# Kernel optimization log

Measured on AMD Instinct MI355X. Metric: run time of the kernel, lower is better.

The kernel has to match this reference:

```python
import jax, jax.numpy as jnp
import numpy as np


def _gcn_conv(x, src, dst, W, b, num_nodes, deg_inv_sqrt):
    # PyG GCNConv: h = x @ W, then normalized scatter-add over edges (incl. self loops), + bias
    h = x @ W  # [N, d_out]
    norm = deg_inv_sqrt[src] * deg_inv_sqrt[dst]  # [E']
    msg = h[src] * norm[:, None]  # gather + scale, [E', d_out]
    out = jax.ops.segment_sum(msg, dst, num_segments=num_nodes)  # scatter-add to targets
    return out + b


def reference(x, edge_index, W1, b1, W2, b2, num_nodes):
    src0, dst0 = edge_index[0], edge_index[1]
    loop = jnp.arange(num_nodes, dtype=edge_index.dtype)
    # add self loops (PyG default add_self_loops=True)
    src = jnp.concatenate([src0, loop])
    dst = jnp.concatenate([dst0, loop])
    # symmetric normalization D^{-1/2} (A+I) D^{-1/2}, degree from self-looped graph
    deg = jax.ops.segment_sum(jnp.ones_like(src, dtype=x.dtype), dst, num_segments=num_nodes)
    deg_inv_sqrt = jnp.where(deg > 0, jax.lax.rsqrt(jnp.maximum(deg, 1)), 0.0).astype(x.dtype)

    z = jax.nn.relu(_gcn_conv(x, src, dst, W1, b1, num_nodes, deg_inv_sqrt))
    z = jax.nn.relu(_gcn_conv(z, src, dst, W2, b2, num_nodes, deg_inv_sqrt))
    return z


def setup_inputs() -> dict:
    key = jax.random.key(0)
    k1, k2, k3, k4 = jax.random.split(key, 4)
    N, E, D, H = 50000, 1600000, 128, 128
    x = jax.random.normal(k1, (N, D), dtype=jnp.float32)
    edge_index = jax.random.randint(k2, (2, E), 0, N, dtype=jnp.int64)
    s = 1.0 / np.sqrt(D)
    W1 = jax.random.normal(k3, (D, H), dtype=jnp.float32) * s
    W2 = jax.random.normal(k4, (H, H), dtype=jnp.float32) * s
    return {
        "x": x,
        "edge_index": edge_index,
        "W1": W1,
        "b1": jnp.zeros((H,), jnp.float32),
        "W2": W2,
        "b2": jnp.zeros((H,), jnp.float32),
        "num_nodes": N,
    }
```

## Files before the change

### kernel.cpp

```cpp
#include <hip/hip_runtime.h>

#define FD 128
#define BSH 7
#define CH 2048
#define CHT 8
#define KMAX 512
#define SCAP 8192

typedef __attribute__((ext_vector_type(8))) short bf16x8;
typedef __attribute__((ext_vector_type(4))) float f32x4;

__device__ inline unsigned bfr(float f) {
    unsigned u = __float_as_uint(f);
    return (u + 0x7FFF + ((u >> 16) & 1)) >> 16;
}
__device__ inline float uplo(unsigned p) { return __uint_as_float(p << 16); }
__device__ inline float uphi(unsigned p) { return __uint_as_float(p & 0xFFFF0000u); }


__global__ __launch_bounds__(256) void partition_kernel(
        const int* __restrict__ src, const int* __restrict__ dst,
        int* __restrict__ lstartG, int* __restrict__ total,
        int* __restrict__ pairs, int E, int K) {
    __shared__ int lcnt[KMAX];
    __shared__ int lstart[KMAX];
    __shared__ int sm[256];
    __shared__ int staged[CH];
    int t = threadIdx.x;
    int base = blockIdx.x * CH;
    int n = min(CH, E - base);

    lcnt[t] = 0; lcnt[t + 256] = 0;
    __syncthreads();

    int pk[CHT]; int bn[CHT];
    #pragma unroll
    for (int j = 0; j < CHT; ++j) {
        int i = t + j * 256;
        bn[j] = -1;
        if (i < n) {
            int d = dst[base + i];
            int s = src[base + i];
            bn[j] = d >> BSH;
            pk[j] = ((d & ((1 << BSH) - 1)) << 17) | s;
            atomicAdd(&lcnt[bn[j]], 1);
        }
    }
    __syncthreads();

    int c0 = lcnt[2 * t], c1 = lcnt[2 * t + 1];
    int s2 = c0 + c1;
    sm[t] = s2;
    __syncthreads();
    for (int off = 1; off < 256; off <<= 1) {
        int add = (t >= off) ? sm[t - off] : 0;
        __syncthreads();
        sm[t] += add;
        __syncthreads();
    }
    int ex = sm[t] - s2;
    lstart[2 * t] = ex;     lstart[2 * t + 1] = ex + c0;
    lcnt[2 * t]   = ex;     lcnt[2 * t + 1]   = ex + c0;
    __syncthreads();

    #pragma unroll
    for (int j = 0; j < CHT; ++j) {
        if (bn[j] >= 0) {
            int pos = atomicAdd(&lcnt[bn[j]], 1);
            staged[pos] = pk[j];
        }
    }
    __syncthreads();

    for (int i = t; i < n; i += 256)
        pairs[base + i] = staged[i];

    size_t lrow = (size_t)blockIdx.x * (K + 1);
    for (int b = t; b < K; b += 256) {
        lstartG[lrow + b] = lstart[b];
        int c = lcnt[b] - lstart[b];
        if (c) atomicAdd(&total[b], c);
    }
    if (t == 0) lstartG[lrow + K] = n;
}

__global__ __launch_bounds__(512) void totscan_kernel(
        const int* __restrict__ total, int* __restrict__ bbase,
        int* __restrict__ rp, int K, int E, int N) {
    __shared__ int sm[512];
    int t = threadIdx.x;
    int v = (t < K) ? total[t] : 0;
    sm[t] = v;
    __syncthreads();
    for (int off = 1; off < 512; off <<= 1) {
        int add = (t >= off) ? sm[t - off] : 0;
        __syncthreads();
        sm[t] += add;
        __syncthreads();
    }
    if (t < K) bbase[t] = sm[t] - v;
    if (t == 0) { bbase[K] = E; rp[N] = E; }
}

__global__ __launch_bounds__(256) void build_kernel(
        const int* __restrict__ pairs, const int* __restrict__ lstartG,
        const int* __restrict__ bbase, int* __restrict__ rp,
        float* __restrict__ dis, int* __restrict__ col, int N, int PB, int K) {
    __shared__ int staged[SCAP];
    __shared__ int lcnt[1 << BSH];
    __shared__ int lsum[1 << BSH];
    __shared__ int lbase[1 << BSH];
    __shared__ int sm[256];
    int b = blockIdx.x;
    int t = threadIdx.x;
    int nbase = b << BSH;
    int nn = min(1 << BSH, N - nbase);
    int beg = bbase[b];
    int cnt = bbase[b + 1] - beg;

    int fp[4], fl0[4], flen[4];
    int nf = 0, mysum = 0;
    for (int p = t; p < PB; p += 256) {
        size_t lrow = (size_t)p * (K + 1);
        int l0 = lstartG[lrow + b];
        int l1 = lstartG[lrow + b + 1];
        fp[nf] = p; fl0[nf] = l0; flen[nf] = l1 - l0;
        mysum += l1 - l0;
        ++nf;
    }
    sm[t] = mysum;
    __syncthreads();
    for (int off = 1; off < 256; off <<= 1) {
        int add = (t >= off) ? sm[t - off] : 0;
        __syncthreads();
        sm[t] += add;
        __syncthreads();
    }
    int o = sm[t] - mysum;

    if (t < 128) lcnt[t] = 0;

    if (cnt <= SCAP) {
        for (int f = 0; f < nf; ++f) {
            int gbase = fp[f] * CH + fl0[f];
            for (int i = 0; i < flen[f]; ++i) staged[o + i] = pairs[gbase + i];
            o += flen[f];
        }
        __syncthreads();
        for (int i = t; i < cnt; i += 256) atomicAdd(&lcnt[staged[i] >> 17], 1);
    } else {
        __syncthreads();
        for (int f = 0; f < nf; ++f) {
            int gbase = fp[f] * CH + fl0[f];
            for (int i = 0; i < flen[f]; ++i)
                atomicAdd(&lcnt[pairs[gbase + i] >> 17], 1);
        }
    }
    __syncthreads();

    if (t < 128) lsum[t] = lcnt[t];
    __syncthreads();
    for (int off = 1; off < 128; off <<= 1) {
        int add = (t < 128 && t >= off) ? lsum[t - off] : 0;
        __syncthreads();
        if (t < 128) lsum[t] += add;
        __syncthreads();
    }
    if (t < 128) {
        int excl = beg + lsum[t] - lcnt[t];
        lbase[t] = excl;
        if (t < nn) {
            rp[nbase + t] = excl;
            dis[nbase + t] = rsqrtf((float)(lcnt[t] + 1));
        }
    }
    __syncthreads();
    if (t < 128) lcnt[t] = lbase[t];
    __syncthreads();

    if (cnt <= SCAP) {
        for (int i = t; i < cnt; i += 256) {
            int p = staged[i];
            int pos = atomicAdd(&lcnt[p >> 17], 1);
            col[pos] = p & 0x1FFFF;
        }
    } else {
        for (int f = 0; f < nf; ++f) {
            int gbase = fp[f] * CH + fl0[f];
            for (int i = 0; i < flen[f]; ++i) {
                int p = pairs[gbase + i];
                int pos = atomicAdd(&lcnt[p >> 17], 1);
                col[pos] = p & 0x1FFFF;
            }
        }
    }
}


__global__ void wt_kernel(const float* __restrict__ W1, unsigned short* __restrict__ W1T,
                          const float* __restrict__ W2, unsigned short* __restrict__ W2T) {
    int k = blockIdx.x & (FD - 1);
    int n = threadIdx.x;
    if (blockIdx.x < FD) W1T[n * FD + k] = (unsigned short)bfr(W1[k * FD + n]);
    else                 W2T[n * FD + k] = (unsigned short)bfr(W2[k * FD + n]);
}


#define APAD 8
#define ASTR (FD + APAD)

template <bool A32>
__device__ void gemm_body(const void* __restrict__ Ap,
                          const unsigned short* __restrict__ WT,
                          const float* __restrict__ dis,
                          unsigned short* __restrict__ C, int M) {
    __shared__ unsigned short As[128 * ASTR];
    __shared__ unsigned short Bs[128 * ASTR];
    int tid = threadIdx.x;
    int lane = tid & 63;
    int wave = tid >> 6;
    int quad = lane >> 4;
    int l16 = lane & 15;
    int rowBase = blockIdx.x * 128;

    #pragma unroll
    for (int p = 0; p < 8; ++p) {
        int r = p * 16 + (tid >> 4);
        int cq = (tid & 15) * 8;
        int gr = rowBase + r;
        uint4 v = make_uint4(0u, 0u, 0u, 0u);
        if (A32) {
            if (gr < M) {
                const float* a = (const float*)Ap + (size_t)gr * FD + cq;
                float4 f0 = *(const float4*)a;
                float4 f1 = *(const float4*)(a + 4);
                v.x = bfr(f0.x) | (bfr(f0.y) << 16);
                v.y = bfr(f0.z) | (bfr(f0.w) << 16);
                v.z = bfr(f1.x) | (bfr(f1.y) << 16);
                v.w = bfr(f1.z) | (bfr(f1.w) << 16);
            }
        } else {
            if (gr < M) v = *(const uint4*)((const unsigned short*)Ap + (size_t)gr * FD + cq);
        }
        *(uint4*)&As[r * ASTR + cq] = v;
        *(uint4*)&Bs[r * ASTR + cq] = *(const uint4*)&WT[(size_t)r * FD + cq];
    }
    __syncthreads();

    int m0 = wave * 32;
    f32x4 acc[2][8] = {};
    #pragma unroll
    for (int kt = 0; kt < 4; ++kt) {
        int ko = kt * 32 + quad * 8;
        bf16x8 a0 = *(bf16x8*)&As[(m0 + l16) * ASTR + ko];
        bf16x8 a1 = *(bf16x8*)&As[(m0 + 16 + l16) * ASTR + ko];
        #pragma unroll
        for (int n = 0; n < 8; ++n) {
            bf16x8 b = *(bf16x8*)&Bs[(n * 16 + l16) * ASTR + ko];
            acc[0][n] = __builtin_amdgcn_mfma_f32_16x16x32_bf16(a0, b, acc[0][n], 0, 0, 0);
            acc[1][n] = __builtin_amdgcn_mfma_f32_16x16x32_bf16(a1, b, acc[1][n], 0, 0, 0);
        }
    }

    #pragma unroll
    for (int ms = 0; ms < 2; ++ms) {
        #pragma unroll
        for (int r = 0; r < 4; ++r) {
            int grow = rowBase + m0 + ms * 16 + quad * 4 + r;
            if (grow < M) {
                float dv = dis[grow];
                #pragma unroll
                for (int n = 0; n < 8; ++n) {
                    C[(size_t)grow * FD + n * 16 + l16] =
                        (unsigned short)bfr(dv * acc[ms][n][r]);
                }
            }
        }
    }
}

__global__ __launch_bounds__(256) void gemm_mfma_f32(
        const float* __restrict__ A, const unsigned short* __restrict__ WT,
        const float* __restrict__ dis, unsigned short* __restrict__ C, int M) {
    gemm_body<true>(A, WT, dis, C, M);
}

__global__ __launch_bounds__(256) void gemm_mfma_bf16(
        const unsigned short* __restrict__ A, const unsigned short* __restrict__ WT,
        const float* __restrict__ dis, unsigned short* __restrict__ C, int M) {
    gemm_body<false>(A, WT, dis, C, M);
}


__global__ __launch_bounds__(256) void agg_kernel(
        const unsigned* __restrict__ h, const float* __restrict__ dis,
        const int* __restrict__ rp, const int* __restrict__ col,
        const float2* __restrict__ bias, void* __restrict__ out, int N, int obf) {
    int v = blockIdx.x * 4 + threadIdx.y;
    v = __builtin_amdgcn_readfirstlane(v);
    if (v >= N) return;
    int t = threadIdx.x;
    float dv = dis[v];
    size_t vb = (size_t)v * 64 + t;
    unsigned hp = h[vb];
    float2 acc;
    acc.x = uplo(hp); acc.y = uphi(hp);
    int e = rp[v];
    int end = rp[v + 1];

    for (; e + 16 <= end; e += 16) {
        int u[16];
        #pragma unroll
        for (int j = 0; j < 16; ++j) u[j] = col[e + j];
        unsigned p[16];
        #pragma unroll
        for (int j = 0; j < 16; ++j) p[j] = h[(size_t)u[j] * 64 + t];
        #pragma unroll
        for (int j = 0; j < 16; ++j) {
            acc.x += uplo(p[j]); acc.y += uphi(p[j]);
        }
    }
    for (; e + 4 <= end; e += 4) {
        int u0 = col[e], u1 = col[e + 1], u2 = col[e + 2], u3 = col[e + 3];
        unsigned p0 = h[(size_t)u0 * 64 + t];
        unsigned p1 = h[(size_t)u1 * 64 + t];
        unsigned p2 = h[(size_t)u2 * 64 + t];
        unsigned p3 = h[(size_t)u3 * 64 + t];
        acc.x += uplo(p0); acc.y += uphi(p0);
        acc.x += uplo(p1); acc.y += uphi(p1);
        acc.x += uplo(p2); acc.y += uphi(p2);
        acc.x += uplo(p3); acc.y += uphi(p3);
    }
    for (; e < end; ++e) {
        unsigned p = h[(size_t)col[e] * 64 + t];
        acc.x += uplo(p); acc.y += uphi(p);
    }

    float2 bb = bias[t];
    float2 r;
    r.x = fmaxf(fmaf(dv, acc.x, bb.x), 0.0f);
    r.y = fmaxf(fmaf(dv, acc.y, bb.y), 0.0f);
    if (obf) {
        ((unsigned*)out)[vb] = bfr(r.x) | (bfr(r.y) << 16);
    } else {
        ((float2*)out)[vb] = r;
    }
}


extern "C" void kernel_launch(void* const* d_in, const int* in_sizes, int n_in,
                              void* d_out, int out_size, void* d_ws, size_t ws_size,
                              hipStream_t stream) {
    const float* x  = (const float*)d_in[0];
    const int*   ei = (const int*)d_in[1];
    const float* W1 = (const float*)d_in[2];
    const float* b1 = (const float*)d_in[3];
    const float* W2 = (const float*)d_in[4];
    const float* b2 = (const float*)d_in[5];

    int N = in_sizes[0] / FD;
    int E = in_sizes[1] / 2;
    const int* src = ei;
    const int* dst = ei + E;
    int K = (N + (1 << BSH) - 1) >> BSH;
    int PB = (E + CH - 1) / CH;

    char* base = (char*)d_ws;
    size_t off = 0;
    auto align256 = [](size_t v) { return (v + 255) & ~(size_t)255; };
    int*            rp    = (int*)(base + off);            off += align256((size_t)(N + 1) * 4);
    float*          dis   = (float*)(base + off);          off += align256((size_t)N * 4);
    int*            total = (int*)(base + off);            off += align256(512 * 4);
    int*            bbase = (int*)(base + off);            off += align256(513 * 4);
    unsigned short* w1t   = (unsigned short*)(base + off); off += align256((size_t)FD * FD * 2);
    unsigned short* w2t   = (unsigned short*)(base + off); off += align256((size_t)FD * FD * 2);
    int*            col   = (int*)(base + off);            off += align256((size_t)E * 4);
    unsigned short* hbuf  = (unsigned short*)(base + off); off += align256((size_t)N * FD * 2);
    unsigned short* z1    = (unsigned short*)(base + off); off += align256((size_t)N * FD * 2);
    int*            pairs = (int*)(base + off);            off += align256((size_t)E * 4);
    int*            lstartG = (int*)hbuf;
    (void)ws_size; (void)n_in; (void)out_size;

    (void)hipMemsetAsync(total, 0, 512 * 4, stream);
    partition_kernel<<<PB, 256, 0, stream>>>(src, dst, lstartG, total, pairs, E, K);
    totscan_kernel  <<<1, 512, 0, stream>>>(total, bbase, rp, K, E, N);
    build_kernel    <<<K, 256, 0, stream>>>(pairs, lstartG, bbase, rp, dis, col, N, PB, K);

    wt_kernel<<<2 * FD, FD, 0, stream>>>(W1, w1t, W2, w2t);

    dim3 aggBlk(64, 4);
    int aggGrid = (N + 3) / 4;
    int gemmGrid = (N + 127) / 128;

    gemm_mfma_f32 <<<gemmGrid, 256, 0, stream>>>(x, w1t, dis, hbuf, N);
    agg_kernel<<<aggGrid, aggBlk, 0, stream>>>((const unsigned*)hbuf, dis, rp, col,
                                               (const float2*)b1, z1, N, 1);
    gemm_mfma_bf16<<<gemmGrid, 256, 0, stream>>>(z1, w2t, dis, hbuf, N);
    agg_kernel<<<aggGrid, aggBlk, 0, stream>>>((const unsigned*)hbuf, dis, rp, col,
                                               (const float2*)b2, d_out, N, 0);
}
```

Measured before the change: 258.1 us.

## Bin CSR edges by source chunk and aggregate chunk-wise over several nodes per wave

The CSR build now sorts each destination row's edges into 8 source-index chunks and records per-chunk row pointers. The aggregation kernel handles 7 nodes per wave and walks the chunks in order, so concurrent gathers of h rows hit a narrower source range for better cache locality. A new transpose kernel makes the build kernel's lstart reads coalesced. In exchange, the per-node inner loops are shorter with less unrolling, there are fewer waves, and an extra rpc array of NCH*N ints is written. The aggregation loop also skips the last chunk, so edges with source index 57344 or above would be dropped; that cannot happen at this N.

```diff
diff --git a/kernel.cpp b/kernel.cpp
--- a/kernel.cpp
+++ b/kernel.cpp
@@ -6,6 +6,9 @@
 #define CHT 8
 #define KMAX 512
 #define SCAP 8192
+#define NCH 8
+#define CSH 13
+#define NPW 7
 
 typedef __attribute__((ext_vector_type(8))) short bf16x8;
 typedef __attribute__((ext_vector_type(4))) float f32x4;
@@ -102,14 +105,30 @@
     if (t == 0) { bbase[K] = E; rp[N] = E; }
 }
 
+__global__ __launch_bounds__(256) void tr_kernel(
+        const int* __restrict__ A, int* __restrict__ B, int R, int C) {
+    __shared__ int tile[32][33];
+    int c0 = blockIdx.x * 32, r0 = blockIdx.y * 32;
+    int tx = threadIdx.x, ty = threadIdx.y;
+    for (int i = ty; i < 32; i += 8) {
+        int r = r0 + i, c = c0 + tx;
+        if (r < R && c < C) tile[i][tx] = A[(size_t)r * C + c];
+    }
+    __syncthreads();
+    for (int i = ty; i < 32; i += 8) {
+        int c = c0 + i, r = r0 + tx;
+        if (c < C && r < R) B[(size_t)c * R + r] = tile[tx][i];
+    }
+}
+
 __global__ __launch_bounds__(256) void build_kernel(
-        const int* __restrict__ pairs, const int* __restrict__ lstartG,
+        const int* __restrict__ pairs, const int* __restrict__ lstartT,
         const int* __restrict__ bbase, int* __restrict__ rp,
-        float* __restrict__ dis, int* __restrict__ col, int N, int PB, int K) {
+        int* __restrict__ rpc, float* __restrict__ dis,
+        int* __restrict__ col, int N, int PB, int K) {
     __shared__ int staged[SCAP];
-    __shared__ int lcnt[1 << BSH];
-    __shared__ int lsum[1 << BSH];
-    __shared__ int lbase[1 << BSH];
+    __shared__ int lcnt[128 * NCH];
+    __shared__ int pref[128 * NCH];
     __shared__ int sm[256];
     int b = blockIdx.x;
     int t = threadIdx.x;
@@ -121,9 +140,8 @@
     int fp[4], fl0[4], flen[4];
     int nf = 0, mysum = 0;
     for (int p = t; p < PB; p += 256) {
-        size_t lrow = (size_t)p * (K + 1);
-        int l0 = lstartG[lrow + b];
-        int l1 = lstartG[lrow + b + 1];
+        int l0 = lstartT[(size_t)b * PB + p];
+        int l1 = lstartT[(size_t)(b + 1) * PB + p];
         fp[nf] = p; fl0[nf] = l0; flen[nf] = l1 - l0;
         mysum += l1 - l0;
         ++nf;
@@ -138,7 +156,7 @@
     }
     int o = sm[t] - mysum;
 
-    if (t < 128) lcnt[t] = 0;
+    lcnt[t] = 0; lcnt[t + 256] = 0; lcnt[t + 512] = 0; lcnt[t + 768] = 0;
 
     if (cnt <= SCAP) {
         for (int f = 0; f < nf; ++f) {
@@ -147,41 +165,62 @@
             o += flen[f];
         }
         __syncthreads();
-        for (int i = t; i < cnt; i += 256) atomicAdd(&lcnt[staged[i] >> 17], 1);
+        for (int i = t; i < cnt; i += 256) {
+            int p = staged[i];
+            atomicAdd(&lcnt[((p >> 17) << 3) | ((p & 0x1FFFF) >> CSH)], 1);
+        }
     } else {
         __syncthreads();
         for (int f = 0; f < nf; ++f) {
             int gbase = fp[f] * CH + fl0[f];
-            for (int i = 0; i < flen[f]; ++i)
-                atomicAdd(&lcnt[pairs[gbase + i] >> 17], 1);
-        }
-    }
-    __syncthreads();
-
-    if (t < 128) lsum[t] = lcnt[t];
-    __syncthreads();
-    for (int off = 1; off < 128; off <<= 1) {
-        int add = (t < 128 && t >= off) ? lsum[t - off] : 0;
-        __syncthreads();
-        if (t < 128) lsum[t] += add;
-        __syncthreads();
-    }
-    if (t < 128) {
-        int excl = beg + lsum[t] - lcnt[t];
-        lbase[t] = excl;
-        if (t < nn) {
-            rp[nbase + t] = excl;
-            dis[nbase + t] = rsqrtf((float)(lcnt[t] + 1));
-        }
-    }
-    __syncthreads();
-    if (t < 128) lcnt[t] = lbase[t];
+            for (int i = 0; i < flen[f]; ++i) {
+                int p = pairs[gbase + i];
+                atomicAdd(&lcnt[((p >> 17) << 3) | ((p & 0x1FFFF) >> CSH)], 1);
+            }
+        }
+    }
+    __syncthreads();
+
+    int b0 = 4 * t;
+    int c0 = lcnt[b0], c1 = lcnt[b0 + 1], c2 = lcnt[b0 + 2], c3 = lcnt[b0 + 3];
+    int s4 = c0 + c1 + c2 + c3;
+    sm[t] = s4;
+    __syncthreads();
+    for (int off = 1; off < 256; off <<= 1) {
+        int add = (t >= off) ? sm[t - off] : 0;
+        __syncthreads();
+        sm[t] += add;
+        __syncthreads();
+    }
+    int ex = sm[t] - s4;
+    pref[b0] = ex; pref[b0 + 1] = ex + c0;
+    pref[b0 + 2] = ex + c0 + c1; pref[b0 + 3] = ex + c0 + c1 + c2;
+    __syncthreads();
+
+    if (t < 128 && t < nn) {
+        int rs = pref[t << 3];
+        int re = (t < 127) ? pref[(t + 1) << 3] : cnt;
+        rp[nbase + t] = beg + rs;
+        dis[nbase + t] = rsqrtf((float)(re - rs + 1));
+    }
+    #pragma unroll
+    for (int j = 0; j < 4; ++j) {
+        int bin = b0 + j;
+        int row = bin >> 3, p = bin & (NCH - 1);
+        if (row < nn) rpc[(size_t)p * N + nbase + row] = beg + pref[bin];
+    }
+    __syncthreads();
+    lcnt[b0]     = beg + pref[b0];
+    lcnt[b0 + 1] = beg + pref[b0 + 1];
+    lcnt[b0 + 2] = beg + pref[b0 + 2];
+    lcnt[b0 + 3] = beg + pref[b0 + 3];
     __syncthreads();
 
     if (cnt <= SCAP) {
         for (int i = t; i < cnt; i += 256) {
             int p = staged[i];
-            int pos = atomicAdd(&lcnt[p >> 17], 1);
+            int key = ((p >> 17) << 3) | ((p & 0x1FFFF) >> CSH);
+            int pos = atomicAdd(&lcnt[key], 1);
             col[pos] = p & 0x1FFFF;
         }
     } else {
@@ -189,7 +228,8 @@
             int gbase = fp[f] * CH + fl0[f];
             for (int i = 0; i < flen[f]; ++i) {
                 int p = pairs[gbase + i];
-                int pos = atomicAdd(&lcnt[p >> 17], 1);
+                int key = ((p >> 17) << 3) | ((p & 0x1FFFF) >> CSH);
+                int pos = atomicAdd(&lcnt[key], 1);
                 col[pos] = p & 0x1FFFF;
             }
         }
@@ -292,58 +332,63 @@
 }
 
 
-__global__ __launch_bounds__(256) void agg_kernel(
+__global__ __launch_bounds__(256, 7) void agg_kernel(
         const unsigned* __restrict__ h, const float* __restrict__ dis,
-        const int* __restrict__ rp, const int* __restrict__ col,
+        const int* __restrict__ rpc, const int* __restrict__ col,
         const float2* __restrict__ bias, void* __restrict__ out, int N, int obf) {
-    int v = blockIdx.x * 4 + threadIdx.y;
-    v = __builtin_amdgcn_readfirstlane(v);
-    if (v >= N) return;
+    int wid = __builtin_amdgcn_readfirstlane(blockIdx.x * 4 + threadIdx.y);
     int t = threadIdx.x;
-    float dv = dis[v];
-    size_t vb = (size_t)v * 64 + t;
-    unsigned hp = h[vb];
-    float2 acc;
-    acc.x = uplo(hp); acc.y = uphi(hp);
-    int e = rp[v];
-    int end = rp[v + 1];
-
-    for (; e + 16 <= end; e += 16) {
-        int u[16];
+    int v0 = wid * NPW;
+    if (v0 >= N) return;
+    int nv = min(NPW, N - v0);
+
+    float2 acc[NPW];
+    #pragma unroll
+    for (int s = 0; s < NPW; ++s) acc[s] = make_float2(0.0f, 0.0f);
+
+    for (int p = 0; p < NCH - 1; ++p) {
+        int st[NPW], en[NPW];
         #pragma unroll
-        for (int j = 0; j < 16; ++j) u[j] = col[e + j];
-        unsigned p[16];
+        for (int s = 0; s < NPW; ++s) {
+            if (s < nv) {
+                st[s] = rpc[(size_t)p * N + v0 + s];
+                en[s] = rpc[(size_t)(p + 1) * N + v0 + s];
+            } else { st[s] = 0; en[s] = 0; }
+        }
         #pragma unroll
-        for (int j = 0; j < 16; ++j) p[j] = h[(size_t)u[j] * 64 + t];
-        #pragma unroll
-        for (int j = 0; j < 16; ++j) {
-            acc.x += uplo(p[j]); acc.y += uphi(p[j]);
-        }
-    }
-    for (; e + 4 <= end; e += 4) {
-        int u0 = col[e], u1 = col[e + 1], u2 = col[e + 2], u3 = col[e + 3];
-        unsigned p0 = h[(size_t)u0 * 64 + t];
-        unsigned p1 = h[(size_t)u1 * 64 + t];
-        unsigned p2 = h[(size_t)u2 * 64 + t];
-        unsigned p3 = h[(size_t)u3 * 64 + t];
-        acc.x += uplo(p0); acc.y += uphi(p0);
-        acc.x += uplo(p1); acc.y += uphi(p1);
-        acc.x += uplo(p2); acc.y += uphi(p2);
-        acc.x += uplo(p3); acc.y += uphi(p3);
-    }
-    for (; e < end; ++e) {
-        unsigned p = h[(size_t)col[e] * 64 + t];
-        acc.x += uplo(p); acc.y += uphi(p);
+        for (int s = 0; s < NPW; ++s) {
+            int e = st[s], end = en[s];
+            for (; e + 4 <= end; e += 4) {
+                int u0 = col[e], u1 = col[e + 1], u2 = col[e + 2], u3 = col[e + 3];
+                unsigned q0 = h[(size_t)u0 * 64 + t];
+                unsigned q1 = h[(size_t)u1 * 64 + t];
+                unsigned q2 = h[(size_t)u2 * 64 + t];
+                unsigned q3 = h[(size_t)u3 * 64 + t];
+                acc[s].x += uplo(q0); acc[s].y += uphi(q0);
+                acc[s].x += uplo(q1); acc[s].y += uphi(q1);
+                acc[s].x += uplo(q2); acc[s].y += uphi(q2);
+                acc[s].x += uplo(q3); acc[s].y += uphi(q3);
+            }
+            for (; e < end; ++e) {
+                unsigned q = h[(size_t)col[e] * 64 + t];
+                acc[s].x += uplo(q); acc[s].y += uphi(q);
+            }
+        }
     }
 
     float2 bb = bias[t];
-    float2 r;
-    r.x = fmaxf(fmaf(dv, acc.x, bb.x), 0.0f);
-    r.y = fmaxf(fmaf(dv, acc.y, bb.y), 0.0f);
-    if (obf) {
-        ((unsigned*)out)[vb] = bfr(r.x) | (bfr(r.y) << 16);
-    } else {
-        ((float2*)out)[vb] = r;
+    #pragma unroll
+    for (int s = 0; s < NPW; ++s) {
+        if (s < nv) {
+            int v = v0 + s;
+            float dv = dis[v];
+            size_t vb = (size_t)v * 64 + t;
+            unsigned hp = h[vb];
+            float rx = fmaxf(fmaf(dv, acc[s].x + uplo(hp), bb.x), 0.0f);
+            float ry = fmaxf(fmaf(dv, acc[s].y + uphi(hp), bb.y), 0.0f);
+            if (obf) ((unsigned*)out)[vb] = bfr(rx) | (bfr(ry) << 16);
+            else     ((float2*)out)[vb] = make_float2(rx, ry);
+        }
     }
 }
 
@@ -378,24 +423,29 @@
     unsigned short* hbuf  = (unsigned short*)(base + off); off += align256((size_t)N * FD * 2);
     unsigned short* z1    = (unsigned short*)(base + off); off += align256((size_t)N * FD * 2);
     int*            pairs = (int*)(base + off);            off += align256((size_t)E * 4);
+    int*            rpc   = (int*)(base + off);            off += align256((size_t)NCH * N * 4);
     int*            lstartG = (int*)hbuf;
+    int*            lstartT = (int*)z1;
     (void)ws_size; (void)n_in; (void)out_size;
 
     (void)hipMemsetAsync(total, 0, 512 * 4, stream);
     partition_kernel<<<PB, 256, 0, stream>>>(src, dst, lstartG, total, pairs, E, K);
     totscan_kernel  <<<1, 512, 0, stream>>>(total, bbase, rp, K, E, N);
-    build_kernel    <<<K, 256, 0, stream>>>(pairs, lstartG, bbase, rp, dis, col, N, PB, K);
+    dim3 trb(32, 8);
+    dim3 trg((K + 1 + 31) / 32, (PB + 31) / 32);
+    tr_kernel       <<<trg, trb, 0, stream>>>(lstartG, lstartT, PB, K + 1);
+    build_kernel    <<<K, 256, 0, stream>>>(pairs, lstartT, bbase, rp, rpc, dis, col, N, PB, K);
 
     wt_kernel<<<2 * FD, FD, 0, stream>>>(W1, w1t, W2, w2t);
 
     dim3 aggBlk(64, 4);
-    int aggGrid = (N + 3) / 4;
+    int aggGrid = (N + 4 * NPW - 1) / (4 * NPW);
     int gemmGrid = (N + 127) / 128;
 
     gemm_mfma_f32 <<<gemmGrid, 256, 0, stream>>>(x, w1t, dis, hbuf, N);
-    agg_kernel<<<aggGrid, aggBlk, 0, stream>>>((const unsigned*)hbuf, dis, rp, col,
+    agg_kernel<<<aggGrid, aggBlk, 0, stream>>>((const unsigned*)hbuf, dis, rpc, col,
                                                (const float2*)b1, z1, N, 1);
     gemm_mfma_bf16<<<gemmGrid, 256, 0, stream>>>(z1, w2t, dis, hbuf, N);
-    agg_kernel<<<aggGrid, aggBlk, 0, stream>>>((const unsigned*)hbuf, dis, rp, col,
+    agg_kernel<<<aggGrid, aggBlk, 0, stream>>>((const unsigned*)hbuf, dis, rpc, col,
                                                (const float2*)b2, d_out, N, 0);
 }
```

Measured after the change: 297.9 us. +15.4%, slower.
